# Kernel tuning notes

Hardware: AMD Instinct MI355X
Metric: run time of the kernel (lower is better)

## Reference

```python
import jax, jax.numpy as jnp
import numpy as np

N, NODE_F, EDGE_F = 50000, 192, 64
M = 800000  # directed edges
D = NODE_F + EDGE_F  # inner_dim = 256
OUT = 2048
DEPTH = 3


def setup_inputs() -> dict:
    key = jax.random.key(0)
    ks = jax.random.split(key, 8)
    node_attr = jax.random.normal(ks[0], (N, NODE_F), dtype=jnp.float32)
    edge_attr = jax.random.normal(ks[1], (M, EDGE_F), dtype=jnp.float32)
    edge_src = jax.random.randint(ks[2], (M,), 0, N, dtype=jnp.int32)
    edge_dst = jax.random.randint(ks[3], (M,), 0, N, dtype=jnp.int32)
    # per-depth parameters (original stacks copies along a depth axis)
    W_inner = jnp.stack([jnp.eye(D, dtype=jnp.float32)
                         + 0.01 * jax.random.normal(jax.random.fold_in(ks[4], d), (D, D))
                         for d in range(DEPTH)])                      # [DEPTH, D, D]
    b_inner = jnp.zeros((DEPTH, D), dtype=jnp.float32)
    scale = jnp.sqrt(6.0 / (D + OUT)).astype(jnp.float32)            # glorot_uniform
    W_output = jax.random.uniform(ks[5], (DEPTH + 1, D, OUT), jnp.float32, -scale, scale)
    b_output = jnp.zeros((DEPTH + 1, OUT), dtype=jnp.float32)
    return {"node_attr": node_attr, "edge_attr": edge_attr,
            "edge_src": edge_src, "edge_dst": edge_dst,
            "W_inner": W_inner, "b_inner": b_inner,
            "W_output": W_output, "b_output": b_output}


def _fp_contribution(attr, W_out_d, b_out_d):
    # softmax over fingerprint dim per node, summed over nodes -> [OUT]
    return jax.nn.softmax(attr @ W_out_d + b_out_d, axis=-1).sum(axis=0)


def reference(node_attr, edge_attr, edge_src, edge_dst,
              W_inner, b_inner, W_output, b_output):
    n = node_attr.shape[0]
    # attributes = [nodeAttributes | zeros(edge_feat)]  -> [N, D]
    attr = jnp.concatenate(
        [node_attr, jnp.zeros((n, edge_attr.shape[1]), node_attr.dtype)], axis=1)
    fp = _fp_contribution(attr, W_output[0], b_output[0])
    # per-edge payload: [zeros(node_feat) | edgeAttr]  -> [M, D]
    edge_pad = jnp.concatenate(
        [jnp.zeros((edge_attr.shape[0], node_attr.shape[1]), edge_attr.dtype), edge_attr],
        axis=1)
    for d in range(1, DEPTH + 1):
        # v_i = attr_i + sum_{(ni,ei) in nbrs(i)} (attr_ni + [0|edgeAttr_ei])
        msgs = attr[edge_src] + edge_pad                 # [M, D] gather
        agg = jax.ops.segment_sum(msgs, edge_dst, num_segments=n)
        v = attr + agg
        # activation_inner = 'linear' (identity)
        attr = v @ W_inner[d - 1] + b_inner[d - 1]
        fp = fp + _fp_contribution(attr, W_output[d], b_output[d])
    return fp  # [OUT]
```

## Files before the change

kernel.cpp:

```cpp
#include <hip/hip_runtime.h>
#include <hip/hip_bf16.h>

#define N_NODES 50000
#define N_PAD   50016
#define NODE_F  192
#define EDGE_F  64
#define DIM     256
#define OUT_DIM 2048
#define DEPTH   3
#define M_EDGES 800000

typedef short  bf16x8 __attribute__((ext_vector_type(8)));
typedef float  f32x4  __attribute__((ext_vector_type(4)));

__device__ inline short f2bf(float f) {
    unsigned u = __float_as_uint(f);
    unsigned r = (u + 0x7fffu + ((u >> 16) & 1u)) >> 16;
    return (short)r;
}

__global__ void k_init_attr(const float* __restrict__ node_attr,
                            float* __restrict__ attr,
                            short* __restrict__ attr_bf) {
    int i = blockIdx.x * 256 + threadIdx.x;
    int row = i >> 6, q = i & 63;
    if (row >= N_PAD) return;
    float4 v = make_float4(0.f, 0.f, 0.f, 0.f);
    if (row < N_NODES && q < NODE_F / 4)
        v = ((const float4*)node_attr)[row * (NODE_F / 4) + q];
    if (row < N_NODES) ((float4*)attr)[i] = v;
    short4 s; s.x = f2bf(v.x); s.y = f2bf(v.y); s.z = f2bf(v.z); s.w = f2bf(v.w);
    ((short4*)attr_bf)[i] = s;
}

__global__ void k_degree(const int* __restrict__ dst, int* __restrict__ deg) {
    int e = blockIdx.x * 256 + threadIdx.x;
    if (e < M_EDGES) atomicAdd(&deg[dst[e]], 1);
}

__global__ __launch_bounds__(1024) void k_scan(int* __restrict__ deg,
                                               int* __restrict__ rowptr) {
    __shared__ int part[1024];
    int t = threadIdx.x;
    const int CH = (N_NODES + 1023) / 1024;
    int beg = t * CH, end = min(beg + CH, N_NODES);
    int s = 0;
    for (int i = beg; i < end; i++) s += deg[i];
    part[t] = s;
    __syncthreads();
    for (int off = 1; off < 1024; off <<= 1) {
        int v = (t >= off) ? part[t - off] : 0;
        __syncthreads();
        part[t] += v;
        __syncthreads();
    }
    int run = (t == 0) ? 0 : part[t - 1];
    for (int i = beg; i < end; i++) {
        int d = deg[i];
        rowptr[i] = run;
        deg[i] = run;
        run += d;
    }
    if (t == 1023) rowptr[N_NODES] = run;
}

__global__ void k_fill(const int* __restrict__ dst, int* __restrict__ cursor,
                       int* __restrict__ eidx) {
    int e = blockIdx.x * 256 + threadIdx.x;
    if (e < M_EDGES) {
        int p = atomicAdd(&cursor[dst[e]], 1);
        eidx[p] = e;
    }
}

__global__ __launch_bounds__(256) void k_gather(const float* __restrict__ attr,
                                                const float* __restrict__ edge_attr,
                                                const int* __restrict__ src,
                                                const int* __restrict__ rowptr,
                                                const int* __restrict__ eidx,
                                                float* __restrict__ agg) {
    int gid = blockIdx.x * 256 + threadIdx.x;
    int node = gid >> 6, q = gid & 63;
    if (node >= N_NODES) return;
    int beg = rowptr[node], end = rowptr[node + 1];
    float4 acc = make_float4(0.f, 0.f, 0.f, 0.f);
    const float4* A4 = (const float4*)attr;
    const float4* E4 = (const float4*)edge_attr;
    for (int i = beg; i < end; i++) {
        int e = eidx[i];
        int s = src[e];
        float4 v = A4[(size_t)s * 64 + q];
        if (q >= NODE_F / 4) {
            float4 ea = E4[(size_t)e * (EDGE_F / 4) + (q - NODE_F / 4)];
            v.x += ea.x; v.y += ea.y; v.z += ea.z; v.w += ea.w;
        }
        acc.x += v.x; acc.y += v.y; acc.z += v.z; acc.w += v.w;
    }
    ((float4*)agg)[(size_t)node * 64 + q] = acc;
}

__global__ __launch_bounds__(256) void k_inner(const float* __restrict__ attr,
                                               const float* __restrict__ agg,
                                               const float* __restrict__ W,
                                               const float* __restrict__ b,
                                               float* __restrict__ out,
                                               short* __restrict__ out_bf) {
    __shared__ float4 sV[32][64];
    int tid  = threadIdx.x;
    int row0 = blockIdx.x * 32;

    for (int i = tid; i < 32 * 64; i += 256) {
        int r = i >> 6, q = i & 63;
        int grow = row0 + r;
        float4 v = make_float4(0.f, 0.f, 0.f, 0.f);
        if (grow < N_NODES) {
            float4 a = ((const float4*)attr)[(size_t)grow * 64 + q];
            float4 g = ((const float4*)agg)[(size_t)grow * 64 + q];
            v = make_float4(a.x + g.x, a.y + g.y, a.z + g.z, a.w + g.w);
        }
        sV[r][q] = v;
    }
    __syncthreads();

    int cg = tid & 63;
    int rg = tid >> 6;

    float4 acc[8];
#pragma unroll
    for (int r = 0; r < 8; r++) acc[r] = make_float4(0.f, 0.f, 0.f, 0.f);

    const float4* W4 = (const float4*)W;
    for (int k4 = 0; k4 < 64; k4++) {
        float4 w0 = W4[(size_t)(k4 * 4 + 0) * 64 + cg];
        float4 w1 = W4[(size_t)(k4 * 4 + 1) * 64 + cg];
        float4 w2 = W4[(size_t)(k4 * 4 + 2) * 64 + cg];
        float4 w3 = W4[(size_t)(k4 * 4 + 3) * 64 + cg];
#pragma unroll
        for (int r = 0; r < 8; r++) {
            float4 a = sV[rg * 8 + r][k4];
            acc[r].x += a.x * w0.x + a.y * w1.x + a.z * w2.x + a.w * w3.x;
            acc[r].y += a.x * w0.y + a.y * w1.y + a.z * w2.y + a.w * w3.y;
            acc[r].z += a.x * w0.z + a.y * w1.z + a.z * w2.z + a.w * w3.z;
            acc[r].w += a.x * w0.w + a.y * w1.w + a.z * w2.w + a.w * w3.w;
        }
    }

    float4 bb = ((const float4*)b)[cg];
#pragma unroll
    for (int r = 0; r < 8; r++) {
        int grow = row0 + rg * 8 + r;
        if (grow < N_NODES) {
            float4 o = make_float4(acc[r].x + bb.x, acc[r].y + bb.y,
                                   acc[r].z + bb.z, acc[r].w + bb.w);
            ((float4*)out)[(size_t)grow * 64 + cg] = o;
            short4 s; s.x = f2bf(o.x); s.y = f2bf(o.y); s.z = f2bf(o.z); s.w = f2bf(o.w);
            ((short4*)out_bf)[(size_t)grow * 64 + cg] = s;
        }
    }
}

__global__ void k_wswz(const float* __restrict__ W, short* __restrict__ Wz) {
    int idx = blockIdx.x * 256 + threadIdx.x;
    int lane = idx & 63;
    int T    = (idx >> 6) & 127;
    int ks   = (idx >> 13) & 7;
    int d    = idx >> 16;
    int quad = lane >> 4;
    int m    = lane & 15;
    const float* src = W + ((size_t)(d * 256 + ks * 32 + quad * 8)) * 2048 + T * 16 + m;
    short* dstp = Wz + (size_t)idx * 8;
#pragma unroll
    for (int j = 0; j < 8; j++) dstp[j] = f2bf(src[(size_t)j * 2048]);
}

__global__ __launch_bounds__(1024)
void k_fp_mfma(const short* __restrict__ attr_bf,
               const short* __restrict__ Wz,
               const float* __restrict__ bias,
               float* __restrict__ fp_part) {
    __shared__ float sred[32][17];
    __shared__ float sfinm[32];
    __shared__ float sfinl[32];
    int tid  = threadIdx.x;
    int lane = tid & 63;
    int wave = tid >> 6;
    int quad = lane >> 4;
    int m    = lane & 15;
    int row0 = blockIdx.x * 32;

    f32x4 acc0[8], acc1[8];
#pragma unroll
    for (int t = 0; t < 8; t++) {
        acc0[t] = (f32x4){0.f, 0.f, 0.f, 0.f};
        acc1[t] = (f32x4){0.f, 0.f, 0.f, 0.f};
    }

    const short* a0p = attr_bf + (size_t)(row0 + m) * 256 + quad * 8;
    const short* a1p = a0p + 16 * 256;
    for (int ks = 0; ks < 8; ks++) {
        bf16x8 af0 = *(const bf16x8*)(a0p + ks * 32);
        bf16x8 af1 = *(const bf16x8*)(a1p + ks * 32);
        const bf16x8* bp = (const bf16x8*)Wz + ((size_t)ks * 128 + wave * 8) * 64 + lane;
#pragma unroll
        for (int t = 0; t < 8; t++) {
            bf16x8 bf = bp[t * 64];
            acc0[t] = __builtin_amdgcn_mfma_f32_16x16x32_bf16(af0, bf, acc0[t], 0, 0, 0);
            acc1[t] = __builtin_amdgcn_mfma_f32_16x16x32_bf16(af1, bf, acc1[t], 0, 0, 0);
        }
    }

#pragma unroll
    for (int t = 0; t < 8; t++) {
        float bb = bias[(wave * 8 + t) * 16 + m];
        acc0[t][0] += bb; acc0[t][1] += bb; acc0[t][2] += bb; acc0[t][3] += bb;
        acc1[t][0] += bb; acc1[t][1] += bb; acc1[t][2] += bb; acc1[t][3] += bb;
    }

    float mx0[4], mx1[4];
#pragma unroll
    for (int r = 0; r < 4; r++) {
        float v0 = acc0[0][r], v1 = acc1[0][r];
#pragma unroll
        for (int t = 1; t < 8; t++) { v0 = fmaxf(v0, acc0[t][r]); v1 = fmaxf(v1, acc1[t][r]); }
        mx0[r] = v0; mx1[r] = v1;
    }
#pragma unroll
    for (int off = 1; off < 16; off <<= 1)
#pragma unroll
        for (int r = 0; r < 4; r++) {
            mx0[r] = fmaxf(mx0[r], __shfl_xor(mx0[r], off));
            mx1[r] = fmaxf(mx1[r], __shfl_xor(mx1[r], off));
        }
    if (m == 0)
#pragma unroll
        for (int r = 0; r < 4; r++) {
            sred[quad * 4 + r][wave]      = mx0[r];
            sred[16 + quad * 4 + r][wave] = mx1[r];
        }
    __syncthreads();
    if (tid < 32) {
        float v = sred[tid][0];
#pragma unroll
        for (int w = 1; w < 16; w++) v = fmaxf(v, sred[tid][w]);
        sfinm[tid] = v;
    }
    __syncthreads();
#pragma unroll
    for (int r = 0; r < 4; r++) { mx0[r] = sfinm[quad * 4 + r]; mx1[r] = sfinm[16 + quad * 4 + r]; }

    float ls0[4] = {0.f, 0.f, 0.f, 0.f}, ls1[4] = {0.f, 0.f, 0.f, 0.f};
#pragma unroll
    for (int t = 0; t < 8; t++) {
#pragma unroll
        for (int r = 0; r < 4; r++) {
            float e0 = __expf(acc0[t][r] - mx0[r]);
            float e1 = __expf(acc1[t][r] - mx1[r]);
            acc0[t][r] = e0; acc1[t][r] = e1;
            ls0[r] += e0; ls1[r] += e1;
        }
    }
#pragma unroll
    for (int off = 1; off < 16; off <<= 1)
#pragma unroll
        for (int r = 0; r < 4; r++) {
            ls0[r] += __shfl_xor(ls0[r], off);
            ls1[r] += __shfl_xor(ls1[r], off);
        }
    if (m == 0)
#pragma unroll
        for (int r = 0; r < 4; r++) {
            sred[quad * 4 + r][wave]      = ls0[r];
            sred[16 + quad * 4 + r][wave] = ls1[r];
        }
    __syncthreads();
    if (tid < 32) {
        float v = 0.f;
#pragma unroll
        for (int w = 0; w < 16; w++) v += sred[tid][w];
        sfinl[tid] = v;
    }
    __syncthreads();

    float rinv0[4], rinv1[4];
#pragma unroll
    for (int r = 0; r < 4; r++) {
        int ra = quad * 4 + r, rb = 16 + quad * 4 + r;
        rinv0[r] = (row0 + ra < N_NODES) ? 1.0f / sfinl[ra] : 0.0f;
        rinv1[r] = (row0 + rb < N_NODES) ? 1.0f / sfinl[rb] : 0.0f;
    }

    float* dst = fp_part + (size_t)(blockIdx.x & 63) * OUT_DIM;
#pragma unroll
    for (int t = 0; t < 8; t++) {
        float cs = acc0[t][0] * rinv0[0] + acc0[t][1] * rinv0[1]
                 + acc0[t][2] * rinv0[2] + acc0[t][3] * rinv0[3]
                 + acc1[t][0] * rinv1[0] + acc1[t][1] * rinv1[1]
                 + acc1[t][2] * rinv1[2] + acc1[t][3] * rinv1[3];
        cs += __shfl_xor(cs, 16);
        cs += __shfl_xor(cs, 32);
        if (quad == 0)
            atomicAdd(&dst[(wave * 8 + t) * 16 + m], cs);
    }
}

__global__ void k_fp_reduce(const float* __restrict__ part, float* __restrict__ fp) {
    int c = blockIdx.x * 256 + threadIdx.x;
    float s = 0.f;
#pragma unroll
    for (int r = 0; r < 64; r++) s += part[(size_t)r * OUT_DIM + c];
    fp[c] = s;
}

extern "C" void kernel_launch(void* const* d_in, const int* in_sizes, int n_in,
                              void* d_out, int out_size, void* d_ws, size_t ws_size,
                              hipStream_t stream) {
    const float* node_attr = (const float*)d_in[0];
    const float* edge_attr = (const float*)d_in[1];
    const int*   edge_src  = (const int*)d_in[2];
    const int*   edge_dst  = (const int*)d_in[3];
    const float* W_inner   = (const float*)d_in[4];
    const float* b_inner   = (const float*)d_in[5];
    const float* W_output  = (const float*)d_in[6];
    const float* b_output  = (const float*)d_in[7];

    float* fp      = (float*)d_out;
    float* attr    = (float*)d_ws;
    float* agg     = attr + (size_t)N_NODES * DIM;
    float* fp_part = agg + (size_t)N_NODES * DIM;
    short* Wz      = (short*)(fp_part + 64 * OUT_DIM);
    int*   deg     = (int*)(Wz + (size_t)4 * 65536 * 8);
    int*   rowptr  = deg + N_NODES;
    int*   eidx    = rowptr + N_NODES + 1;
    short* attr_bf = (short*)(eidx + M_EDGES);

    hipMemsetAsync(fp_part, 0, 64 * OUT_DIM * sizeof(float), stream);
    hipMemsetAsync(deg, 0, N_NODES * sizeof(int), stream);

    k_init_attr<<<(N_PAD * 64 + 255) / 256, 256, 0, stream>>>(node_attr, attr, attr_bf);

    k_degree<<<(M_EDGES + 255) / 256, 256, 0, stream>>>(edge_dst, deg);
    k_scan<<<1, 1024, 0, stream>>>(deg, rowptr);
    k_fill<<<(M_EDGES + 255) / 256, 256, 0, stream>>>(edge_dst, deg, eidx);

    k_wswz<<<1024, 256, 0, stream>>>(W_output, Wz);

    k_fp_mfma<<<N_PAD / 32, 1024, 0, stream>>>(attr_bf, Wz, b_output, fp_part);

    for (int d = 1; d <= DEPTH; d++) {
        k_gather<<<(N_NODES * 64 + 255) / 256, 256, 0, stream>>>(
            attr, edge_attr, edge_src, rowptr, eidx, agg);
        k_inner<<<(N_NODES + 31) / 32, 256, 0, stream>>>(
            attr, agg, W_inner + (size_t)(d - 1) * DIM * DIM,
            b_inner + (size_t)(d - 1) * DIM, attr, attr_bf);
        k_fp_mfma<<<N_PAD / 32, 1024, 0, stream>>>(
            attr_bf, Wz + (size_t)d * 65536 * 8,
            b_output + (size_t)d * OUT_DIM, fp_part);
    }
    k_fp_reduce<<<OUT_DIM / 256, 256, 0, stream>>>(fp_part, fp);
}
```

Before: 2.034 ms.

## Precompute per-node edge-attribute sums and CSR-ordered sources once outside depth loop

Edge attributes are constant across depths, so their per-destination sum is computed once in a new kernel and added as the initial accumulator, instead of gathering edge_attr per edge at every depth. Source indices are also stored in CSR order during fill, which removes the double indirection eidx→src inside the gather loop. This cuts repeated random reads of edge_attr (800k×64 floats per depth). In exchange it adds one extra kernel and workspace for esum and srcs.

```diff
diff --git a/kernel.cpp b/kernel.cpp
--- a/kernel.cpp
+++ b/kernel.cpp
@@ -64,36 +64,51 @@
     if (t == 1023) rowptr[N_NODES] = run;
 }
 
-__global__ void k_fill(const int* __restrict__ dst, int* __restrict__ cursor,
-                       int* __restrict__ eidx) {
+__global__ void k_fill(const int* __restrict__ dst, const int* __restrict__ src,
+                       int* __restrict__ cursor,
+                       int* __restrict__ eidx, int* __restrict__ srcs) {
     int e = blockIdx.x * 256 + threadIdx.x;
     if (e < M_EDGES) {
         int p = atomicAdd(&cursor[dst[e]], 1);
         eidx[p] = e;
-    }
+        srcs[p] = src[e];
+    }
+}
+
+__global__ __launch_bounds__(256) void k_esum(const float* __restrict__ edge_attr,
+                                              const int* __restrict__ rowptr,
+                                              const int* __restrict__ eidx,
+                                              float* __restrict__ esum) {
+    int gid = blockIdx.x * 256 + threadIdx.x;
+    int node = gid >> 4, q = gid & 15;
+    if (node >= N_NODES) return;
+    int beg = rowptr[node], end = rowptr[node + 1];
+    float4 acc = make_float4(0.f, 0.f, 0.f, 0.f);
+    const float4* E4 = (const float4*)edge_attr;
+    for (int i = beg; i < end; i++) {
+        int e = eidx[i];
+        float4 v = E4[(size_t)e * 16 + q];
+        acc.x += v.x; acc.y += v.y; acc.z += v.z; acc.w += v.w;
+    }
+    ((float4*)esum)[(size_t)node * 16 + q] = acc;
 }
 
 __global__ __launch_bounds__(256) void k_gather(const float* __restrict__ attr,
-                                                const float* __restrict__ edge_attr,
-                                                const int* __restrict__ src,
                                                 const int* __restrict__ rowptr,
-                                                const int* __restrict__ eidx,
+                                                const int* __restrict__ srcs,
+                                                const float* __restrict__ esum,
                                                 float* __restrict__ agg) {
     int gid = blockIdx.x * 256 + threadIdx.x;
     int node = gid >> 6, q = gid & 63;
     if (node >= N_NODES) return;
     int beg = rowptr[node], end = rowptr[node + 1];
     float4 acc = make_float4(0.f, 0.f, 0.f, 0.f);
+    if (q >= NODE_F / 4)
+        acc = ((const float4*)esum)[(size_t)node * 16 + (q - NODE_F / 4)];
     const float4* A4 = (const float4*)attr;
-    const float4* E4 = (const float4*)edge_attr;
     for (int i = beg; i < end; i++) {
-        int e = eidx[i];
-        int s = src[e];
+        int s = srcs[i];
         float4 v = A4[(size_t)s * 64 + q];
-        if (q >= NODE_F / 4) {
-            float4 ea = E4[(size_t)e * (EDGE_F / 4) + (q - NODE_F / 4)];
-            v.x += ea.x; v.y += ea.y; v.z += ea.z; v.w += ea.w;
-        }
         acc.x += v.x; acc.y += v.y; acc.z += v.z; acc.w += v.w;
     }
     ((float4*)agg)[(size_t)node * 64 + q] = acc;
@@ -331,7 +346,9 @@
     int*   deg     = (int*)(Wz + (size_t)4 * 65536 * 8);
     int*   rowptr  = deg + N_NODES;
     int*   eidx    = rowptr + N_NODES + 1;
-    short* attr_bf = (short*)(eidx + M_EDGES);
+    int*   srcs    = eidx + M_EDGES;
+    float* esum    = (float*)(srcs + M_EDGES);
+    short* attr_bf = (short*)(esum + (size_t)N_NODES * EDGE_F);
 
     hipMemsetAsync(fp_part, 0, 64 * OUT_DIM * sizeof(float), stream);
     hipMemsetAsync(deg, 0, N_NODES * sizeof(int), stream);
@@ -340,7 +357,8 @@
 
     k_degree<<<(M_EDGES + 255) / 256, 256, 0, stream>>>(edge_dst, deg);
     k_scan<<<1, 1024, 0, stream>>>(deg, rowptr);
-    k_fill<<<(M_EDGES + 255) / 256, 256, 0, stream>>>(edge_dst, deg, eidx);
+    k_fill<<<(M_EDGES + 255) / 256, 256, 0, stream>>>(edge_dst, edge_src, deg, eidx, srcs);
+    k_esum<<<(N_NODES * 16 + 255) / 256, 256, 0, stream>>>(edge_attr, rowptr, eidx, esum);
 
     k_wswz<<<1024, 256, 0, stream>>>(W_output, Wz);
 
@@ -348,7 +366,7 @@
 
     for (int d = 1; d <= DEPTH; d++) {
         k_gather<<<(N_NODES * 64 + 255) / 256, 256, 0, stream>>>(
-            attr, edge_attr, edge_src, rowptr, eidx, agg);
+            attr, rowptr, srcs, esum, agg);
         k_inner<<<(N_NODES + 31) / 32, 256, 0, stream>>>(
             attr, agg, W_inner + (size_t)(d - 1) * DIM * DIM,
             b_inner + (size_t)(d - 1) * DIM, attr, attr_bf);
```

After: 1.859 ms. 1.09x faster.
